# Kernel tuning notes

Measured on AMD Instinct MI355X. Metric: run time of the kernel, lower is better.

## Reference

```python
import math
import jax, jax.numpy as jnp
import numpy as np

D_COMPLEX = 256
KAN_HIDDEN = 32
N_TRANSFORMS = 10  # max_levels=None -> 10 stacked PolarizingBlocks, indexed min(level, 9)


def setup_inputs() -> dict:
    key = jax.random.key(0)
    k1, k2, k3 = jax.random.split(key, 3)
    batch, seq_len, d = 8, 16384, D_COMPLEX
    Z = jax.random.normal(k1, (batch, seq_len, d), dtype=jnp.float32)
    # PolarizingBlock ~ Linear(d, kan_hidden) -> GELU -> Linear(kan_hidden, d)
    s1 = 1.0 / math.sqrt(d)
    s2 = 1.0 / math.sqrt(KAN_HIDDEN)
    W1 = jax.random.normal(k2, (N_TRANSFORMS, d, KAN_HIDDEN), dtype=jnp.float32) * s1
    b1 = jnp.zeros((N_TRANSFORMS, KAN_HIDDEN), dtype=jnp.float32)
    W2 = jax.random.normal(k3, (N_TRANSFORMS, KAN_HIDDEN, d), dtype=jnp.float32) * s2
    b2 = jnp.zeros((N_TRANSFORMS, d), dtype=jnp.float32)
    return {"Z": Z, "W1": W1, "b1": b1, "W2": W2, "b2": b2}


def _polarize(Z, W1, b1, W2, b2):
    batch, seq_len, d = Z.shape  # seq_len is a power of 2
    n_levels = int(math.log2(seq_len))
    for level in range(n_levels):  # fixed small loop over log2(seq) levels
        group_size = 2 ** (level + 1)
        n_groups = seq_len // group_size
        Zg = Z.reshape(batch, n_groups, group_size, d)
        A = Zg.mean(axis=2)  # (batch, n_groups, d) group mean aggregation
        t = min(level, N_TRANSFORMS - 1)
        h = jax.nn.gelu(jnp.einsum("bgd,dh->bgh", A, W1[t]) + b1[t])
        At = jnp.einsum("bgh,hd->bgd", h, W2[t]) + b2[t]
        Z = (Zg + At[:, :, None, :]).reshape(batch, seq_len, d)  # broadcast back
    return Z


def reference(Z, W1, b1, W2, b2):
    return _polarize(Z, W1, b1, W2, b2)
```

## Files before the change

kernel.cpp:

```cpp
#include <hip/hip_runtime.h>


__device__ __forceinline__ float gelu_t(float x){
  float t = tanhf(0.7978845608028654f * (x + 0.044715f * x * x * x));
  return 0.5f * x * (1.0f + t);
}

#define SA 260

__global__ void __launch_bounds__(256) k_fused(
    const float* __restrict__ Z, float* __restrict__ P,
    const float* __restrict__ W1, const float* __restrict__ B1,
    const float* __restrict__ W2, const float* __restrict__ B2)
{
  __shared__ __align__(16) float a_s[32 * SA];
  __shared__ __align__(16) float w_s[8192];
  __shared__ __align__(16) float h_s[32 * 34];
  __shared__ __align__(16) float b1s[32];
  __shared__ __align__(16) float b2s[256];
  const int tid = threadIdx.x;
  const long arow0 = (long)blockIdx.x * 32;

  {
    const float* Zb = Z + (arow0 << 9);
    for(int c = tid; c < 2048; c += 256){
      int r = c >> 6, q = (c & 63) << 2;
      float4 x = *(const float4*)(Zb + ((long)r << 9) + q);
      float4 y = *(const float4*)(Zb + ((long)r << 9) + 256 + q);
      float4 o;
      o.x = 0.5f*(x.x + y.x); o.y = 0.5f*(x.y + y.y);
      o.z = 0.5f*(x.z + y.z); o.w = 0.5f*(x.w + y.w);
      *(float4*)&a_s[r * SA + q] = o;
    }
  }

  int nr = 32;
  for(int l = 0; l < 5; l++){
    const float* W1g = W1 + ((long)l << 13);
    const float* B1g = B1 + (l << 5);
    const float* W2g = W2 + ((long)l << 13);
    const float* B2g = B2 + (l << 8);
    const long Prow = (long)(131072 - (131072 >> l)) + (arow0 >> l);

    for(int c = tid; c < 2048; c += 256)
      *(float4*)&w_s[c << 2] = *(const float4*)(W1g + (c << 2));
    if(tid < 32) b1s[tid] = B1g[tid];
    b2s[tid] = B2g[tid];
    __syncthreads();

    for(int task = tid; task < (nr << 3); task += 256){
      int r = task >> 3, j4 = (task & 7) << 2;
      float4 acc = *(const float4*)&b1s[j4];
      const float4* ap = (const float4*)&a_s[r * SA];
      #pragma unroll 4
      for(int d4 = 0; d4 < 64; d4++){
        float4 a = ap[d4];
        const float* wb = &w_s[(d4 << 7) + j4];
        float4 w0 = *(const float4*)(wb);
        float4 w1 = *(const float4*)(wb + 32);
        float4 w2 = *(const float4*)(wb + 64);
        float4 w3 = *(const float4*)(wb + 96);
        acc.x += a.x*w0.x + a.y*w1.x + a.z*w2.x + a.w*w3.x;
        acc.y += a.x*w0.y + a.y*w1.y + a.z*w2.y + a.w*w3.y;
        acc.z += a.x*w0.z + a.y*w1.z + a.z*w2.z + a.w*w3.z;
        acc.w += a.x*w0.w + a.y*w1.w + a.z*w2.w + a.w*w3.w;
      }
      h_s[(j4+0)*34 + r] = gelu_t(acc.x);
      h_s[(j4+1)*34 + r] = gelu_t(acc.y);
      h_s[(j4+2)*34 + r] = gelu_t(acc.z);
      h_s[(j4+3)*34 + r] = gelu_t(acc.w);
    }
    __syncthreads();

    for(int c = tid; c < 2048; c += 256)
      *(float4*)&w_s[c << 2] = *(const float4*)(W2g + (c << 2));
    __syncthreads();

    const int npair = nr >> 1;
    const int ntask = npair << 6;
    float4 m[4];
    #pragma unroll
    for(int it = 0; it < 4; it++){
      int task = tid + (it << 8);
      if(task < ntask){
        int rp = task >> 6, d4 = (task & 63) << 2;
        int r0 = rp << 1;
        float4 acc0 = *(const float4*)&b2s[d4];
        float4 acc1 = acc0;
        #pragma unroll 4
        for(int j = 0; j < 32; j++){
          float2 hh = *(const float2*)&h_s[j*34 + r0];
          float4 w  = *(const float4*)&w_s[(j << 8) + d4];
          acc0.x += hh.x*w.x; acc0.y += hh.x*w.y;
          acc0.z += hh.x*w.z; acc0.w += hh.x*w.w;
          acc1.x += hh.y*w.x; acc1.y += hh.y*w.y;
          acc1.z += hh.y*w.z; acc1.w += hh.y*w.w;
        }
        *(float4*)(P + ((Prow + r0)     << 8) + d4) = acc0;
        *(float4*)(P + ((Prow + r0 + 1) << 8) + d4) = acc1;
        float4 A0 = *(const float4*)&a_s[ r0    * SA + d4];
        float4 A1 = *(const float4*)&a_s[(r0+1) * SA + d4];
        m[it].x = 0.5f*(A0.x + acc0.x + A1.x + acc1.x);
        m[it].y = 0.5f*(A0.y + acc0.y + A1.y + acc1.y);
        m[it].z = 0.5f*(A0.z + acc0.z + A1.z + acc1.z);
        m[it].w = 0.5f*(A0.w + acc0.w + A1.w + acc1.w);
      }
    }
    __syncthreads();

    if(l < 4){
      #pragma unroll
      for(int it = 0; it < 4; it++){
        int task = tid + (it << 8);
        if(task < ntask){
          int rp = task >> 6, d4 = (task & 63) << 2;
          *(float4*)&a_s[rp * SA + d4] = m[it];
        }
      }
    } else if(tid < 64){
      long p5 = (((long)126976 + blockIdx.x) << 8) + (tid << 2);
      *(float4*)(P + p5) = m[0];
    }
    nr >>= 1;
  }
}

__global__ void __launch_bounds__(512) k_tail(
    float* __restrict__ P,
    const float* __restrict__ W1, const float* __restrict__ B1,
    const float* __restrict__ W2, const float* __restrict__ B2,
    int l0, int l1, int ss)
{
  __shared__ float h_s[128 * 33];
  __shared__ __align__(16) float w1s[8192];
  __shared__ __align__(16) float w2s[8192];
  const int tid = threadIdx.x;
  const int b   = blockIdx.x >> ss;
  const int sub = blockIdx.x & ((1 << ss) - 1);

  for(int l = l0; l <= l1; l++){
    int t = (l < 9) ? l : 9;
    const float* W1g = W1 + ((long)t << 13);
    const float* B1g = B1 + (t << 5);
    const float* W2g = W2 + ((long)t << 13);
    const float* B2g = B2 + (t << 8);
    for(int c = tid; c < 2048; c += 512){
      *(float4*)&w1s[c << 2] = *(const float4*)(W1g + (c << 2));
      *(float4*)&w2s[c << 2] = *(const float4*)(W2g + (c << 2));
    }
    __syncthreads();

    int nbb = 8192 >> l;
    int nbs = nbb >> ss;
    long rowA = (long)(131072 - (131072 >> l)) + (long)b * nbb + (long)sub * nbs;
    float* A = P + (rowA << 8);

    for(int task = tid; task < (nbs << 3); task += 512){
      int r = task >> 3, j4 = (task & 7) << 2;
      float4 acc = *(const float4*)(B1g + j4);
      const float4* ap = (const float4*)(A + ((long)r << 8));
      #pragma unroll 4
      for(int d4 = 0; d4 < 64; d4++){
        float4 a = ap[d4];
        const float* wr = &w1s[(d4 << 7) + j4];
        float4 w0 = *(const float4*)(wr);
        float4 w1 = *(const float4*)(wr + 32);
        float4 w2 = *(const float4*)(wr + 64);
        float4 w3 = *(const float4*)(wr + 96);
        acc.x += a.x*w0.x + a.y*w1.x + a.z*w2.x + a.w*w3.x;
        acc.y += a.x*w0.y + a.y*w1.y + a.z*w2.y + a.w*w3.y;
        acc.z += a.x*w0.z + a.y*w1.z + a.z*w2.z + a.w*w3.z;
        acc.w += a.x*w0.w + a.y*w1.w + a.z*w2.w + a.w*w3.w;
      }
      int hb = r * 33 + j4;
      h_s[hb+0] = gelu_t(acc.x); h_s[hb+1] = gelu_t(acc.y);
      h_s[hb+2] = gelu_t(acc.z); h_s[hb+3] = gelu_t(acc.w);
    }
    __syncthreads();

    int pairs = nbs >> 1;
    if(pairs){
      long rowN = (long)(131072 - (131072 >> (l+1))) + (long)b * (nbb >> 1) + (long)sub * pairs;
      float* An = P + (rowN << 8);
      for(int task = tid; task < (pairs << 5); task += 512){
        int rp = task >> 5, d8 = (task & 31) << 3;
        int r0 = rp << 1, r1 = r0 | 1;
        float* a0 = A + ((long)r0 << 8) + d8;
        float* a1 = A + ((long)r1 << 8) + d8;
        float4 o0a = *(const float4*)(a0), o0b = *(const float4*)(a0 + 4);
        float4 o1a = *(const float4*)(a1), o1b = *(const float4*)(a1 + 4);
        float acc0[8], acc1[8];
        #pragma unroll
        for(int k = 0; k < 8; k++){ float bb = B2g[d8 + k]; acc0[k] = bb; acc1[k] = bb; }
        #pragma unroll 4
        for(int j = 0; j < 32; j++){
          float h0 = h_s[r0*33 + j], h1 = h_s[r1*33 + j];
          const float* wr = &w2s[(j << 8) + d8];
          float4 wa = *(const float4*)(wr);
          float4 wb = *(const float4*)(wr + 4);
          acc0[0] += h0*wa.x; acc0[1] += h0*wa.y; acc0[2] += h0*wa.z; acc0[3] += h0*wa.w;
          acc0[4] += h0*wb.x; acc0[5] += h0*wb.y; acc0[6] += h0*wb.z; acc0[7] += h0*wb.w;
          acc1[0] += h1*wa.x; acc1[1] += h1*wa.y; acc1[2] += h1*wa.z; acc1[3] += h1*wa.w;
          acc1[4] += h1*wb.x; acc1[5] += h1*wb.y; acc1[6] += h1*wb.z; acc1[7] += h1*wb.w;
        }
        *(float4*)(a0)     = make_float4(acc0[0], acc0[1], acc0[2], acc0[3]);
        *(float4*)(a0 + 4) = make_float4(acc0[4], acc0[5], acc0[6], acc0[7]);
        *(float4*)(a1)     = make_float4(acc1[0], acc1[1], acc1[2], acc1[3]);
        *(float4*)(a1 + 4) = make_float4(acc1[4], acc1[5], acc1[6], acc1[7]);
        float4 ma, mb;
        ma.x = 0.5f*(o0a.x + acc0[0] + o1a.x + acc1[0]);
        ma.y = 0.5f*(o0a.y + acc0[1] + o1a.y + acc1[1]);
        ma.z = 0.5f*(o0a.z + acc0[2] + o1a.z + acc1[2]);
        ma.w = 0.5f*(o0a.w + acc0[3] + o1a.w + acc1[3]);
        mb.x = 0.5f*(o0b.x + acc0[4] + o1b.x + acc1[4]);
        mb.y = 0.5f*(o0b.y + acc0[5] + o1b.y + acc1[5]);
        mb.z = 0.5f*(o0b.z + acc0[6] + o1b.z + acc1[6]);
        mb.w = 0.5f*(o0b.w + acc0[7] + o1b.w + acc1[7]);
        *(float4*)(An + ((long)rp << 8) + d8)     = ma;
        *(float4*)(An + ((long)rp << 8) + d8 + 4) = mb;
      }
    } else if(tid < 32){
      int d8 = tid << 3;
      float acc0[8];
      #pragma unroll
      for(int k = 0; k < 8; k++) acc0[k] = B2g[d8 + k];
      #pragma unroll 4
      for(int j = 0; j < 32; j++){
        float h0 = h_s[j];
        const float* wr = &w2s[(j << 8) + d8];
        float4 wa = *(const float4*)(wr);
        float4 wb = *(const float4*)(wr + 4);
        acc0[0] += h0*wa.x; acc0[1] += h0*wa.y; acc0[2] += h0*wa.z; acc0[3] += h0*wa.w;
        acc0[4] += h0*wb.x; acc0[5] += h0*wb.y; acc0[6] += h0*wb.z; acc0[7] += h0*wb.w;
      }
      *(float4*)(A + d8)     = make_float4(acc0[0], acc0[1], acc0[2], acc0[3]);
      *(float4*)(A + d8 + 4) = make_float4(acc0[4], acc0[5], acc0[6], acc0[7]);
    }
    __syncthreads();
  }
}

__global__ void __launch_bounds__(256) k_final(const float* __restrict__ Z,
                                               const float* __restrict__ P,
                                               float* __restrict__ out){
  long t = (long)blockIdx.x * 256 + threadIdx.x;
  long base = t * 4;
  long row  = base >> 8;
  int  doff = (int)(base & 255);
  int  b = (int)(row >> 14), s = (int)(row & 16383);
  float4 acc = *(const float4*)(Z + base);
  #pragma unroll
  for(int l = 0; l < 14; l++){
    int rowoff = 131072 - (131072 >> l);
    int g = s >> (l + 1);
    long p = ((long)(rowoff + (b << (13 - l)) + g) << 8) + doff;
    float4 f = *(const float4*)(P + p);
    acc.x += f.x; acc.y += f.y; acc.z += f.z; acc.w += f.w;
  }
  *(float4*)(out + base) = acc;
}

extern "C" void kernel_launch(void* const* d_in, const int* in_sizes, int n_in,
                              void* d_out, int out_size, void* d_ws, size_t ws_size,
                              hipStream_t stream) {
  const float* Z  = (const float*)d_in[0];
  const float* W1 = (const float*)d_in[1];
  const float* B1 = (const float*)d_in[2];
  const float* W2 = (const float*)d_in[3];
  const float* B2 = (const float*)d_in[4];

  const size_t pyr_elems = 33552384;
  const bool   use_ws    = ws_size >= pyr_elems * sizeof(float);
  float* P = use_ws ? (float*)d_ws : (float*)d_out;

  k_fused<<<2048, 256, 0, stream>>>(Z, P, W1, B1, W2, B2);
  k_tail<<<16, 512, 0, stream>>>(P, W1, B1, W2, B2, 5, 11, 1);
  k_tail<<<8,  512, 0, stream>>>(P, W1, B1, W2, B2, 12, 13, 0);

  if(use_ws){
    k_final<<<32768, 256, 0, stream>>>(Z, P, (float*)d_out);
  }else{
    k_final<<<32768, 256, 0, stream>>>(Z, P, (float*)d_in[0]);
    hipMemcpyAsync(d_out, d_in[0], (size_t)out_size * sizeof(float),
                   hipMemcpyDeviceToDevice, stream);
  }
}
```

Baseline: 598.2 us.

## Accumulate low-level corrections in shared memory and pre-sum coarse levels

The fused up-sweep kernel now handles 16 rows per block over 4 levels. Instead of writing each level's correction to a separate pyramid row, it accumulates levels 0-3 into a per-row delta buffer in shared memory. A new k_dsum kernel pre-sums levels 4-13 per group of 32 sequence positions, so k_final reads only two rows instead of fourteen. The pyramid is shrunk and weights are packed to bf16 in LDS, with the first matmul split across two threads per output. The goal is less global traffic in the final pass and a better tail split, at the cost of bf16 weight precision and an extra launch.

New measurement: 702.4 us. 17.4% more time.

```diff
diff --git a/kernel.cpp b/kernel.cpp
--- a/kernel.cpp
+++ b/kernel.cpp
@@ -6,122 +6,175 @@
   return 0.5f * x * (1.0f + t);
 }
 
+__device__ __forceinline__ unsigned pack_bf2(float a, float b){
+  unsigned ua = __float_as_uint(a); ua = (ua + 0x7fffu + ((ua >> 16) & 1u)) >> 16;
+  unsigned ub = __float_as_uint(b); ub = (ub + 0x7fffu + ((ub >> 16) & 1u)) & 0xffff0000u;
+  return ua | ub;
+}
+
 #define SA 260
-
-__global__ void __launch_bounds__(256) k_fused(
+#define WS 130
+
+__global__ void __launch_bounds__(256) k_up(
     const float* __restrict__ Z, float* __restrict__ P,
     const float* __restrict__ W1, const float* __restrict__ B1,
     const float* __restrict__ W2, const float* __restrict__ B2)
 {
-  __shared__ __align__(16) float a_s[32 * SA];
-  __shared__ __align__(16) float w_s[8192];
-  __shared__ __align__(16) float h_s[32 * 34];
-  __shared__ __align__(16) float b1s[32];
-  __shared__ __align__(16) float b2s[256];
+  __shared__ __align__(16) float a_s[16 * SA];
+  __shared__ __align__(16) float D_s[16 * SA];
+  __shared__ __align__(8)  unsigned w1p[32 * WS];
+  __shared__ __align__(8)  unsigned w2p[32 * WS];
+  __shared__ __align__(8)  float hp0[32 * 18];
+  __shared__ __align__(8)  float hp1[32 * 18];
+  __shared__ float b1s[32];
+  __shared__ float b2s[256];
   const int tid = threadIdx.x;
-  const long arow0 = (long)blockIdx.x * 32;
+  const long arow0 = (long)blockIdx.x * 16;
 
   {
     const float* Zb = Z + (arow0 << 9);
-    for(int c = tid; c < 2048; c += 256){
+    for(int c = tid; c < 1024; c += 256){
       int r = c >> 6, q = (c & 63) << 2;
       float4 x = *(const float4*)(Zb + ((long)r << 9) + q);
       float4 y = *(const float4*)(Zb + ((long)r << 9) + 256 + q);
       float4 o;
-      o.x = 0.5f*(x.x + y.x); o.y = 0.5f*(x.y + y.y);
-      o.z = 0.5f*(x.z + y.z); o.w = 0.5f*(x.w + y.w);
+      o.x = 0.5f*(x.x+y.x); o.y = 0.5f*(x.y+y.y);
+      o.z = 0.5f*(x.z+y.z); o.w = 0.5f*(x.w+y.w);
       *(float4*)&a_s[r * SA + q] = o;
     }
   }
 
-  int nr = 32;
-  for(int l = 0; l < 5; l++){
+  float4 m0 = make_float4(0,0,0,0), m1 = make_float4(0,0,0,0);
+  int nr = 16;
+  for(int l = 0; l < 4; l++){
+    if(l > 0){
+      int ntp = 1024 >> l;
+      if(tid < ntp){
+        int rp = tid >> 6, d0 = (tid & 63) << 2;
+        *(float4*)&a_s[rp * SA + d0] = m0;
+      }
+      if(tid + 256 < ntp){
+        int rp = (tid + 256) >> 6, d0 = (tid & 63) << 2;
+        *(float4*)&a_s[rp * SA + d0] = m1;
+      }
+    }
     const float* W1g = W1 + ((long)l << 13);
-    const float* B1g = B1 + (l << 5);
     const float* W2g = W2 + ((long)l << 13);
-    const float* B2g = B2 + (l << 8);
-    const long Prow = (long)(131072 - (131072 >> l)) + (arow0 >> l);
-
-    for(int c = tid; c < 2048; c += 256)
-      *(float4*)&w_s[c << 2] = *(const float4*)(W1g + (c << 2));
-    if(tid < 32) b1s[tid] = B1g[tid];
-    b2s[tid] = B2g[tid];
-    __syncthreads();
-
-    for(int task = tid; task < (nr << 3); task += 256){
-      int r = task >> 3, j4 = (task & 7) << 2;
-      float4 acc = *(const float4*)&b1s[j4];
-      const float4* ap = (const float4*)&a_s[r * SA];
+    for(int c = tid; c < 4096; c += 256){
+      int j = c & 31, d2 = c >> 5;
+      w1p[j * WS + d2] = pack_bf2(W1g[d2*64 + j], W1g[d2*64 + 32 + j]);
+    }
+    for(int c = tid; c < 4096; c += 256){
+      int d2 = c & 127, j = c >> 7;
+      float2 wv = *(const float2*)(W2g + j*256 + 2*d2);
+      w2p[j * WS + d2] = pack_bf2(wv.x, wv.y);
+    }
+    if(tid < 32) b1s[tid] = B1[(l << 5) + tid];
+    b2s[tid] = B2[(l << 8) + tid];
+    __syncthreads();
+
+    if(tid < (nr << 3)){
+      int dh = tid & 1, jg = (tid >> 1) & 7, rt = tid >> 4;
+      int r0 = rt * 2, r1 = r0 + 1;
+      float acc[2][4];
+      #pragma unroll
+      for(int jj = 0; jj < 4; jj++){
+        float b = dh ? 0.f : b1s[jg*4 + jj];
+        acc[0][jj] = b; acc[1][jj] = b;
+      }
+      const float4* pa0 = (const float4*)&a_s[r0 * SA];
+      const float4* pa1 = (const float4*)&a_s[r1 * SA];
+      const int d4b = dh << 5;
       #pragma unroll 4
-      for(int d4 = 0; d4 < 64; d4++){
-        float4 a = ap[d4];
-        const float* wb = &w_s[(d4 << 7) + j4];
-        float4 w0 = *(const float4*)(wb);
-        float4 w1 = *(const float4*)(wb + 32);
-        float4 w2 = *(const float4*)(wb + 64);
-        float4 w3 = *(const float4*)(wb + 96);
-        acc.x += a.x*w0.x + a.y*w1.x + a.z*w2.x + a.w*w3.x;
-        acc.y += a.x*w0.y + a.y*w1.y + a.z*w2.y + a.w*w3.y;
-        acc.z += a.x*w0.z + a.y*w1.z + a.z*w2.z + a.w*w3.z;
-        acc.w += a.x*w0.w + a.y*w1.w + a.z*w2.w + a.w*w3.w;
-      }
-      h_s[(j4+0)*34 + r] = gelu_t(acc.x);
-      h_s[(j4+1)*34 + r] = gelu_t(acc.y);
-      h_s[(j4+2)*34 + r] = gelu_t(acc.z);
-      h_s[(j4+3)*34 + r] = gelu_t(acc.w);
-    }
-    __syncthreads();
-
-    for(int c = tid; c < 2048; c += 256)
-      *(float4*)&w_s[c << 2] = *(const float4*)(W2g + (c << 2));
-    __syncthreads();
-
-    const int npair = nr >> 1;
-    const int ntask = npair << 6;
-    float4 m[4];
-    #pragma unroll
-    for(int it = 0; it < 4; it++){
-      int task = tid + (it << 8);
-      if(task < ntask){
-        int rp = task >> 6, d4 = (task & 63) << 2;
-        int r0 = rp << 1;
-        float4 acc0 = *(const float4*)&b2s[d4];
-        float4 acc1 = acc0;
-        #pragma unroll 4
-        for(int j = 0; j < 32; j++){
-          float2 hh = *(const float2*)&h_s[j*34 + r0];
-          float4 w  = *(const float4*)&w_s[(j << 8) + d4];
-          acc0.x += hh.x*w.x; acc0.y += hh.x*w.y;
-          acc0.z += hh.x*w.z; acc0.w += hh.x*w.w;
-          acc1.x += hh.y*w.x; acc1.y += hh.y*w.y;
-          acc1.z += hh.y*w.z; acc1.w += hh.y*w.w;
+      for(int dd = 0; dd < 32; dd++){
+        int d4 = d4b + dd;
+        float4 a0 = pa0[d4], a1 = pa1[d4];
+        #pragma unroll
+        for(int jj = 0; jj < 4; jj++){
+          uint2 u = *(const uint2*)&w1p[(jg*4 + jj) * WS + 2*d4];
+          float wa = __uint_as_float(u.x << 16);
+          float wb = __uint_as_float(u.x & 0xffff0000u);
+          float wc = __uint_as_float(u.y << 16);
+          float wd = __uint_as_float(u.y & 0xffff0000u);
+          acc[0][jj] += a0.x*wa + a0.y*wb + a0.z*wc + a0.w*wd;
+          acc[1][jj] += a1.x*wa + a1.y*wb + a1.z*wc + a1.w*wd;
         }
-        *(float4*)(P + ((Prow + r0)     << 8) + d4) = acc0;
-        *(float4*)(P + ((Prow + r0 + 1) << 8) + d4) = acc1;
-        float4 A0 = *(const float4*)&a_s[ r0    * SA + d4];
-        float4 A1 = *(const float4*)&a_s[(r0+1) * SA + d4];
-        m[it].x = 0.5f*(A0.x + acc0.x + A1.x + acc1.x);
-        m[it].y = 0.5f*(A0.y + acc0.y + A1.y + acc1.y);
-        m[it].z = 0.5f*(A0.z + acc0.z + A1.z + acc1.z);
-        m[it].w = 0.5f*(A0.w + acc0.w + A1.w + acc1.w);
-      }
-    }
-    __syncthreads();
-
-    if(l < 4){
+      }
+      float* hp = dh ? hp1 : hp0;
       #pragma unroll
-      for(int it = 0; it < 4; it++){
-        int task = tid + (it << 8);
-        if(task < ntask){
-          int rp = task >> 6, d4 = (task & 63) << 2;
-          *(float4*)&a_s[rp * SA + d4] = m[it];
+      for(int jj = 0; jj < 4; jj++){
+        hp[(jg*4 + jj)*18 + r0] = acc[0][jj];
+        hp[(jg*4 + jj)*18 + r1] = acc[1][jj];
+      }
+    }
+    __syncthreads();
+
+    {
+      int ne = nr << 5;
+      for(int e = tid; e < ne; e += 256){
+        int r = e >> 5, j = e & 31;
+        hp0[j*18 + r] = gelu_t(hp0[j*18 + r] + hp1[j*18 + r]);
+      }
+    }
+    __syncthreads();
+
+    const int ntask = (nr >> 1) << 6;
+    auto at_body = [&](int task) -> float4 {
+      int rp = task >> 6, d0 = (task & 63) << 2;
+      float4 acc0 = *(const float4*)&b2s[d0];
+      float4 acc1 = acc0;
+      #pragma unroll 4
+      for(int j = 0; j < 32; j++){
+        float2 hh = *(const float2*)&hp0[j*18 + 2*rp];
+        uint2 u = *(const uint2*)&w2p[j * WS + (d0 >> 1)];
+        float wa = __uint_as_float(u.x << 16);
+        float wb = __uint_as_float(u.x & 0xffff0000u);
+        float wc = __uint_as_float(u.y << 16);
+        float wd = __uint_as_float(u.y & 0xffff0000u);
+        acc0.x += hh.x*wa; acc0.y += hh.x*wb; acc0.z += hh.x*wc; acc0.w += hh.x*wd;
+        acc1.x += hh.y*wa; acc1.y += hh.y*wb; acc1.z += hh.y*wc; acc1.w += hh.y*wd;
+      }
+      int r0 = rp*2, r1 = r0 + 1;
+      int span = 1 << l;
+      for(int i = 0; i < span; i++){
+        float* dp = &D_s[((r0 << l) + i) * SA + d0];
+        float* dq = &D_s[((r1 << l) + i) * SA + d0];
+        if(l == 0){
+          *(float4*)dp = acc0;
+          *(float4*)dq = acc1;
+        }else{
+          float4 dv = *(const float4*)dp;
+          dv.x += acc0.x; dv.y += acc0.y; dv.z += acc0.z; dv.w += acc0.w;
+          *(float4*)dp = dv;
+          float4 ev = *(const float4*)dq;
+          ev.x += acc1.x; ev.y += acc1.y; ev.z += acc1.z; ev.w += acc1.w;
+          *(float4*)dq = ev;
         }
       }
-    } else if(tid < 64){
-      long p5 = (((long)126976 + blockIdx.x) << 8) + (tid << 2);
-      *(float4*)(P + p5) = m[0];
-    }
+      float4 A0v = *(const float4*)&a_s[r0 * SA + d0];
+      float4 A1v = *(const float4*)&a_s[r1 * SA + d0];
+      float4 mm;
+      mm.x = 0.5f*(A0v.x + acc0.x + A1v.x + acc1.x);
+      mm.y = 0.5f*(A0v.y + acc0.y + A1v.y + acc1.y);
+      mm.z = 0.5f*(A0v.z + acc0.z + A1v.z + acc1.z);
+      mm.w = 0.5f*(A0v.w + acc0.w + A1v.w + acc1.w);
+      return mm;
+    };
+    if(tid < ntask){
+      m0 = at_body(tid);
+      if(l == 3){
+        int d0 = (tid & 63) << 2;
+        *(float4*)(P + (((long)65536 + blockIdx.x) << 8) + d0) = m0;
+      }
+    }
+    if(tid + 256 < ntask) m1 = at_body(tid + 256);
+    __syncthreads();
     nr >>= 1;
+  }
+
+  for(int c = tid; c < 1024; c += 256){
+    int r = c >> 6, q = (c & 63) << 2;
+    *(float4*)(P + ((arow0 + r) << 8) + q) = *(const float4*)&D_s[r * SA + q];
   }
 }
 
@@ -131,7 +184,7 @@
     const float* __restrict__ W2, const float* __restrict__ B2,
     int l0, int l1, int ss)
 {
-  __shared__ float h_s[128 * 33];
+  __shared__ float h_s[64 * 33];
   __shared__ __align__(16) float w1s[8192];
   __shared__ __align__(16) float w2s[8192];
   const int tid = threadIdx.x;
@@ -152,7 +205,7 @@
 
     int nbb = 8192 >> l;
     int nbs = nbb >> ss;
-    long rowA = (long)(131072 - (131072 >> l)) + (long)b * nbb + (long)sub * nbs;
+    long rowA = (long)(73728 - (131072 >> l)) + (long)b * nbb + (long)sub * nbs;
     float* A = P + (rowA << 8);
 
     for(int task = tid; task < (nbs << 3); task += 512){
@@ -180,7 +233,7 @@
 
     int pairs = nbs >> 1;
     if(pairs){
-      long rowN = (long)(131072 - (131072 >> (l+1))) + (long)b * (nbb >> 1) + (long)sub * pairs;
+      long rowN = (long)(73728 - (131072 >> (l+1))) + (long)b * (nbb >> 1) + (long)sub * pairs;
       float* An = P + (rowN << 8);
       for(int task = tid; task < (pairs << 5); task += 512){
         int rp = task >> 5, d8 = (task & 31) << 3;
@@ -240,6 +293,21 @@
   }
 }
 
+__global__ void __launch_bounds__(256) k_dsum(float* __restrict__ P){
+  long idx = (long)blockIdx.x * 256 + threadIdx.x;
+  int g  = (int)(idx >> 6);
+  int d0 = (int)(idx & 63) << 2;
+  int b = g >> 9, gb = g & 511;
+  float4 acc = make_float4(0.f, 0.f, 0.f, 0.f);
+  #pragma unroll
+  for(int l = 4; l < 14; l++){
+    long row = (long)(73728 - (131072 >> l)) + ((long)b << (13 - l)) + (gb >> (l - 4));
+    float4 f = *(const float4*)(P + (row << 8) + d0);
+    acc.x += f.x; acc.y += f.y; acc.z += f.z; acc.w += f.w;
+  }
+  *(float4*)(P + ((long)(73720 + g) << 8) + d0) = acc;
+}
+
 __global__ void __launch_bounds__(256) k_final(const float* __restrict__ Z,
                                                const float* __restrict__ P,
                                                float* __restrict__ out){
@@ -249,14 +317,12 @@
   int  doff = (int)(base & 255);
   int  b = (int)(row >> 14), s = (int)(row & 16383);
   float4 acc = *(const float4*)(Z + base);
-  #pragma unroll
-  for(int l = 0; l < 14; l++){
-    int rowoff = 131072 - (131072 >> l);
-    int g = s >> (l + 1);
-    long p = ((long)(rowoff + (b << (13 - l)) + g) << 8) + doff;
-    float4 f = *(const float4*)(P + p);
-    acc.x += f.x; acc.y += f.y; acc.z += f.z; acc.w += f.w;
-  }
+  long drow = ((long)b << 13) + (s >> 1);
+  float4 dv = *(const float4*)(P + (drow << 8) + doff);
+  long srow = 73720 + ((long)b << 9) + (s >> 5);
+  float4 sv = *(const float4*)(P + (srow << 8) + doff);
+  acc.x += dv.x + sv.x; acc.y += dv.y + sv.y;
+  acc.z += dv.z + sv.z; acc.w += dv.w + sv.w;
   *(float4*)(out + base) = acc;
 }
 
@@ -269,13 +335,14 @@
   const float* W2 = (const float*)d_in[3];
   const float* B2 = (const float*)d_in[4];
 
-  const size_t pyr_elems = 33552384;
+  const size_t pyr_elems = (size_t)77816 * 256;
   const bool   use_ws    = ws_size >= pyr_elems * sizeof(float);
   float* P = use_ws ? (float*)d_ws : (float*)d_out;
 
-  k_fused<<<2048, 256, 0, stream>>>(Z, P, W1, B1, W2, B2);
-  k_tail<<<16, 512, 0, stream>>>(P, W1, B1, W2, B2, 5, 11, 1);
-  k_tail<<<8,  512, 0, stream>>>(P, W1, B1, W2, B2, 12, 13, 0);
+  k_up<<<4096, 256, 0, stream>>>(Z, P, W1, B1, W2, B2);
+  k_tail<<<64, 512, 0, stream>>>(P, W1, B1, W2, B2, 4, 9, 3);
+  k_tail<<<8,  512, 0, stream>>>(P, W1, B1, W2, B2, 10, 13, 0);
+  k_dsum<<<1024, 256, 0, stream>>>(P);
 
   if(use_ws){
     k_final<<<32768, 256, 0, stream>>>(Z, P, (float*)d_out);
```

## Split fused pyramid kernel, split-K first GEMM, pre-sum deep levels for final pass

Applied to the files above, without the earlier changes.

The single fused kernel for levels 0-4 becomes two launches, levels 0-1 and 2-4, so the later levels run with more active threads per block. The first matmul is split across two half-K partial buffers that are summed before GELU, and each thread now computes two or four rows to raise reuse of loaded weights. A new small kernel folds pyramid levels 6-13 into level 5 ahead of time, so the final broadcast pass reads 6 levels instead of 14. In exchange the intermediate level-2 means take an extra round trip through global memory and there are two more launches.

Result: faster. 526.7 us (-12.0%).

```diff
diff --git a/kernel.cpp b/kernel.cpp
--- a/kernel.cpp
+++ b/kernel.cpp
@@ -7,120 +7,162 @@
 }
 
 #define SA 260
-
-__global__ void __launch_bounds__(256) k_fused(
+#define HS 36
+
+__global__ void __launch_bounds__(256) k_block(
     const float* __restrict__ Z, float* __restrict__ P,
     const float* __restrict__ W1, const float* __restrict__ B1,
-    const float* __restrict__ W2, const float* __restrict__ B2)
+    const float* __restrict__ W2, const float* __restrict__ B2,
+    int l_base, int n_lev)
 {
   __shared__ __align__(16) float a_s[32 * SA];
   __shared__ __align__(16) float w_s[8192];
-  __shared__ __align__(16) float h_s[32 * 34];
-  __shared__ __align__(16) float b1s[32];
-  __shared__ __align__(16) float b2s[256];
+  __shared__ __align__(16) float hp0[32 * HS];
+  __shared__ __align__(16) float hp1[32 * HS];
+  __shared__ float b1s[32];
+  __shared__ float b2s[256];
   const int tid = threadIdx.x;
-  const long arow0 = (long)blockIdx.x * 32;
-
-  {
-    const float* Zb = Z + (arow0 << 9);
+  const long g0 = (long)blockIdx.x * 32;
+
+  if(l_base == 0){
+    const float* Zb = Z + (g0 << 9);
     for(int c = tid; c < 2048; c += 256){
       int r = c >> 6, q = (c & 63) << 2;
       float4 x = *(const float4*)(Zb + ((long)r << 9) + q);
       float4 y = *(const float4*)(Zb + ((long)r << 9) + 256 + q);
       float4 o;
-      o.x = 0.5f*(x.x + y.x); o.y = 0.5f*(x.y + y.y);
-      o.z = 0.5f*(x.z + y.z); o.w = 0.5f*(x.w + y.w);
+      o.x = 0.5f*(x.x+y.x); o.y = 0.5f*(x.y+y.y);
+      o.z = 0.5f*(x.z+y.z); o.w = 0.5f*(x.w+y.w);
       *(float4*)&a_s[r * SA + q] = o;
     }
-  }
-
+  }else{
+    const float* Ab = P + (((long)(131072 - (131072 >> l_base)) + g0) << 8);
+    for(int c = tid; c < 2048; c += 256){
+      int r = c >> 6, q = (c & 63) << 2;
+      *(float4*)&a_s[r * SA + q] = *(const float4*)(Ab + ((long)r << 8) + q);
+    }
+  }
+
+  float4 mA[2], mB[2];
+  int ntask_prev = 0;
   int nr = 32;
-  for(int l = 0; l < 5; l++){
+  for(int i = 0; i < n_lev; i++){
+    const int l = l_base + i;
     const float* W1g = W1 + ((long)l << 13);
-    const float* B1g = B1 + (l << 5);
     const float* W2g = W2 + ((long)l << 13);
-    const float* B2g = B2 + (l << 8);
-    const long Prow = (long)(131072 - (131072 >> l)) + (arow0 >> l);
-
+
+    if(i > 0){
+      #pragma unroll
+      for(int it = 0; it < 2; it++){
+        int task = tid + (it << 8);
+        if(task < ntask_prev){
+          int pp = task >> 6, d0 = (task & 63) << 2;
+          *(float4*)&a_s[(2*pp    ) * SA + d0] = mA[it];
+          *(float4*)&a_s[(2*pp + 1) * SA + d0] = mB[it];
+        }
+      }
+    }
     for(int c = tid; c < 2048; c += 256)
       *(float4*)&w_s[c << 2] = *(const float4*)(W1g + (c << 2));
-    if(tid < 32) b1s[tid] = B1g[tid];
-    b2s[tid] = B2g[tid];
-    __syncthreads();
-
-    for(int task = tid; task < (nr << 3); task += 256){
-      int r = task >> 3, j4 = (task & 7) << 2;
-      float4 acc = *(const float4*)&b1s[j4];
-      const float4* ap = (const float4*)&a_s[r * SA];
+    if(tid < 32) b1s[tid] = B1[(l << 5) + tid];
+    b2s[tid] = B2[(l << 8) + tid];
+    __syncthreads();
+
+    if(tid < (nr << 3)){
+      int dh = tid & 1, jg = (tid >> 1) & 7, rt = tid >> 4;
+      int r0 = rt * 2, r1 = r0 + 1;
+      float acc0[4], acc1[4];
+      #pragma unroll
+      for(int jj = 0; jj < 4; jj++){
+        float b = dh ? 0.f : b1s[jg*4 + jj];
+        acc0[jj] = b; acc1[jj] = b;
+      }
+      const float4* pa0 = (const float4*)&a_s[r0 * SA];
+      const float4* pa1 = (const float4*)&a_s[r1 * SA];
+      const int db = dh << 5;
       #pragma unroll 4
-      for(int d4 = 0; d4 < 64; d4++){
-        float4 a = ap[d4];
-        const float* wb = &w_s[(d4 << 7) + j4];
+      for(int dd = 0; dd < 32; dd++){
+        int d4 = db + dd;
+        float4 a0 = pa0[d4], a1 = pa1[d4];
+        const float* wb = &w_s[(d4 << 7) + (jg << 2)];
         float4 w0 = *(const float4*)(wb);
         float4 w1 = *(const float4*)(wb + 32);
         float4 w2 = *(const float4*)(wb + 64);
         float4 w3 = *(const float4*)(wb + 96);
-        acc.x += a.x*w0.x + a.y*w1.x + a.z*w2.x + a.w*w3.x;
-        acc.y += a.x*w0.y + a.y*w1.y + a.z*w2.y + a.w*w3.y;
-        acc.z += a.x*w0.z + a.y*w1.z + a.z*w2.z + a.w*w3.z;
-        acc.w += a.x*w0.w + a.y*w1.w + a.z*w2.w + a.w*w3.w;
-      }
-      h_s[(j4+0)*34 + r] = gelu_t(acc.x);
-      h_s[(j4+1)*34 + r] = gelu_t(acc.y);
-      h_s[(j4+2)*34 + r] = gelu_t(acc.z);
-      h_s[(j4+3)*34 + r] = gelu_t(acc.w);
+        acc0[0] += a0.x*w0.x + a0.y*w1.x + a0.z*w2.x + a0.w*w3.x;
+        acc0[1] += a0.x*w0.y + a0.y*w1.y + a0.z*w2.y + a0.w*w3.y;
+        acc0[2] += a0.x*w0.z + a0.y*w1.z + a0.z*w2.z + a0.w*w3.z;
+        acc0[3] += a0.x*w0.w + a0.y*w1.w + a0.z*w2.w + a0.w*w3.w;
+        acc1[0] += a1.x*w0.x + a1.y*w1.x + a1.z*w2.x + a1.w*w3.x;
+        acc1[1] += a1.x*w0.y + a1.y*w1.y + a1.z*w2.y + a1.w*w3.y;
+        acc1[2] += a1.x*w0.z + a1.y*w1.z + a1.z*w2.z + a1.w*w3.z;
+        acc1[3] += a1.x*w0.w + a1.y*w1.w + a1.z*w2.w + a1.w*w3.w;
+      }
+      float* hp = dh ? hp1 : hp0;
+      #pragma unroll
+      for(int jj = 0; jj < 4; jj++){
+        hp[(jg*4 + jj)*HS + r0] = acc0[jj];
+        hp[(jg*4 + jj)*HS + r1] = acc1[jj];
+      }
     }
     __syncthreads();
 
     for(int c = tid; c < 2048; c += 256)
       *(float4*)&w_s[c << 2] = *(const float4*)(W2g + (c << 2));
-    __syncthreads();
-
-    const int npair = nr >> 1;
-    const int ntask = npair << 6;
-    float4 m[4];
+    for(int e = tid; e < (nr << 5); e += 256){
+      int r = e >> 5, j = e & 31;
+      hp0[j*HS + r] = gelu_t(hp0[j*HS + r] + hp1[j*HS + r]);
+    }
+    __syncthreads();
+
+    const long Prow  = (long)(131072 - (131072 >> l)) + (g0 >> i);
+    const long ProwN = (long)(131072 - (131072 >> (l+1))) + (g0 >> (i+1));
+    const int  npp   = nr >> 2;
+    const int  ntask = npp << 6;
+    const bool last  = (i == n_lev - 1);
     #pragma unroll
-    for(int it = 0; it < 4; it++){
+    for(int it = 0; it < 2; it++){
       int task = tid + (it << 8);
       if(task < ntask){
-        int rp = task >> 6, d4 = (task & 63) << 2;
-        int r0 = rp << 1;
-        float4 acc0 = *(const float4*)&b2s[d4];
-        float4 acc1 = acc0;
+        int pp = task >> 6, d0 = (task & 63) << 2;
+        int q0 = pp << 2;
+        float4 bb = *(const float4*)&b2s[d0];
+        float4 acc0 = bb, acc1 = bb, acc2 = bb, acc3 = bb;
         #pragma unroll 4
         for(int j = 0; j < 32; j++){
-          float2 hh = *(const float2*)&h_s[j*34 + r0];
-          float4 w  = *(const float4*)&w_s[(j << 8) + d4];
-          acc0.x += hh.x*w.x; acc0.y += hh.x*w.y;
-          acc0.z += hh.x*w.z; acc0.w += hh.x*w.w;
-          acc1.x += hh.y*w.x; acc1.y += hh.y*w.y;
-          acc1.z += hh.y*w.z; acc1.w += hh.y*w.w;
+          float4 hh = *(const float4*)&hp0[j*HS + q0];
+          float4 w  = *(const float4*)&w_s[(j << 8) + d0];
+          acc0.x += hh.x*w.x; acc0.y += hh.x*w.y; acc0.z += hh.x*w.z; acc0.w += hh.x*w.w;
+          acc1.x += hh.y*w.x; acc1.y += hh.y*w.y; acc1.z += hh.y*w.z; acc1.w += hh.y*w.w;
+          acc2.x += hh.z*w.x; acc2.y += hh.z*w.y; acc2.z += hh.z*w.z; acc2.w += hh.z*w.w;
+          acc3.x += hh.w*w.x; acc3.y += hh.w*w.y; acc3.z += hh.w*w.z; acc3.w += hh.w*w.w;
         }
-        *(float4*)(P + ((Prow + r0)     << 8) + d4) = acc0;
-        *(float4*)(P + ((Prow + r0 + 1) << 8) + d4) = acc1;
-        float4 A0 = *(const float4*)&a_s[ r0    * SA + d4];
-        float4 A1 = *(const float4*)&a_s[(r0+1) * SA + d4];
-        m[it].x = 0.5f*(A0.x + acc0.x + A1.x + acc1.x);
-        m[it].y = 0.5f*(A0.y + acc0.y + A1.y + acc1.y);
-        m[it].z = 0.5f*(A0.z + acc0.z + A1.z + acc1.z);
-        m[it].w = 0.5f*(A0.w + acc0.w + A1.w + acc1.w);
-      }
-    }
-    __syncthreads();
-
-    if(l < 4){
-      #pragma unroll
-      for(int it = 0; it < 4; it++){
-        int task = tid + (it << 8);
-        if(task < ntask){
-          int rp = task >> 6, d4 = (task & 63) << 2;
-          *(float4*)&a_s[rp * SA + d4] = m[it];
+        *(float4*)(P + ((Prow + q0    ) << 8) + d0) = acc0;
+        *(float4*)(P + ((Prow + q0 + 1) << 8) + d0) = acc1;
+        *(float4*)(P + ((Prow + q0 + 2) << 8) + d0) = acc2;
+        *(float4*)(P + ((Prow + q0 + 3) << 8) + d0) = acc3;
+        float4 A0 = *(const float4*)&a_s[(q0    ) * SA + d0];
+        float4 A1 = *(const float4*)&a_s[(q0 + 1) * SA + d0];
+        float4 A2 = *(const float4*)&a_s[(q0 + 2) * SA + d0];
+        float4 A3 = *(const float4*)&a_s[(q0 + 3) * SA + d0];
+        float4 ma, mb;
+        ma.x = 0.5f*(A0.x + acc0.x + A1.x + acc1.x);
+        ma.y = 0.5f*(A0.y + acc0.y + A1.y + acc1.y);
+        ma.z = 0.5f*(A0.z + acc0.z + A1.z + acc1.z);
+        ma.w = 0.5f*(A0.w + acc0.w + A1.w + acc1.w);
+        mb.x = 0.5f*(A2.x + acc2.x + A3.x + acc3.x);
+        mb.y = 0.5f*(A2.y + acc2.y + A3.y + acc3.y);
+        mb.z = 0.5f*(A2.z + acc2.z + A3.z + acc3.z);
+        mb.w = 0.5f*(A2.w + acc2.w + A3.w + acc3.w);
+        mA[it] = ma; mB[it] = mb;
+        if(last){
+          *(float4*)(P + ((ProwN + 2*pp    ) << 8) + d0) = ma;
+          *(float4*)(P + ((ProwN + 2*pp + 1) << 8) + d0) = mb;
         }
       }
-    } else if(tid < 64){
-      long p5 = (((long)126976 + blockIdx.x) << 8) + (tid << 2);
-      *(float4*)(P + p5) = m[0];
-    }
+    }
+    __syncthreads();
+    ntask_prev = ntask;
     nr >>= 1;
   }
 }
@@ -240,6 +282,24 @@
   }
 }
 
+__global__ void __launch_bounds__(256) k_dsum(float* __restrict__ P){
+  long idx = (long)blockIdx.x * 256 + threadIdx.x;
+  int g  = (int)(idx >> 6);
+  int d0 = (int)(idx & 63) << 2;
+  int b = g >> 8, gb = g & 255;
+  float4 acc = make_float4(0.f, 0.f, 0.f, 0.f);
+  #pragma unroll
+  for(int l = 6; l < 14; l++){
+    long row = (long)(131072 - (131072 >> l)) + ((long)b << (13 - l)) + (gb >> (l - 5));
+    float4 f = *(const float4*)(P + (row << 8) + d0);
+    acc.x += f.x; acc.y += f.y; acc.z += f.z; acc.w += f.w;
+  }
+  float* p5 = P + (((long)126976 + g) << 8) + d0;
+  float4 v = *(const float4*)p5;
+  v.x += acc.x; v.y += acc.y; v.z += acc.z; v.w += acc.w;
+  *(float4*)p5 = v;
+}
+
 __global__ void __launch_bounds__(256) k_final(const float* __restrict__ Z,
                                                const float* __restrict__ P,
                                                float* __restrict__ out){
@@ -250,7 +310,7 @@
   int  b = (int)(row >> 14), s = (int)(row & 16383);
   float4 acc = *(const float4*)(Z + base);
   #pragma unroll
-  for(int l = 0; l < 14; l++){
+  for(int l = 0; l < 6; l++){
     int rowoff = 131072 - (131072 >> l);
     int g = s >> (l + 1);
     long p = ((long)(rowoff + (b << (13 - l)) + g) << 8) + doff;
@@ -273,9 +333,11 @@
   const bool   use_ws    = ws_size >= pyr_elems * sizeof(float);
   float* P = use_ws ? (float*)d_ws : (float*)d_out;
 
-  k_fused<<<2048, 256, 0, stream>>>(Z, P, W1, B1, W2, B2);
+  k_block<<<2048, 256, 0, stream>>>(Z, P, W1, B1, W2, B2, 0, 2);
+  k_block<<<512,  256, 0, stream>>>(Z, P, W1, B1, W2, B2, 2, 3);
   k_tail<<<16, 512, 0, stream>>>(P, W1, B1, W2, B2, 5, 11, 1);
   k_tail<<<8,  512, 0, stream>>>(P, W1, B1, W2, B2, 12, 13, 0);
+  k_dsum<<<512, 256, 0, stream>>>(P);
 
   if(use_ws){
     k_final<<<32768, 256, 0, stream>>>(Z, P, (float*)d_out);
```
